# Performance work log

Hardware: AMD Instinct MI355X
Metric: run time of the kernel (lower is better)

The kernel has to match this reference:

```python
import jax, jax.numpy as jnp
from jax import lax
import numpy as np

KS = 5
STRIDE = 4
SCALE = 10.0
PAD = 1        # conv_transpose2d padding (hardcoded in source)
OUT_PAD = 1    # output_padding
DN = ('NCHW', 'OIHW', 'NCHW')


def _same_pad(x, ks, stride):
    # torch same_padding: pad so out = ceil(H/stride)
    H, W = x.shape[-2], x.shape[-1]
    oh = -(-H // stride); ow = -(-W // stride)
    ph = max(0, (oh - 1) * stride + ks - H)
    pw = max(0, (ow - 1) * stride + ks - W)
    return jnp.pad(x, ((0, 0), (0, 0), (ph // 2, ph - ph // 2), (pw // 2, pw - pw // 2)))


def _patches(x, ks, stride):
    # torch extract_image_patches (same padding + unfold), returned as [N, L, C, ks, ks]
    N, C, H, W = x.shape
    oh = -(-H // stride); ow = -(-W // stride)
    xp = _same_pad(x, ks, stride)
    ys = (jnp.arange(oh) * stride)[:, None] + jnp.arange(ks)[None, :]   # [oh, ks]
    xs = (jnp.arange(ow) * stride)[:, None] + jnp.arange(ks)[None, :]   # [ow, ks]
    p = xp[:, :, ys, :][:, :, :, :, xs]   # [N, C, oh, ks, ow, ks]
    return p.transpose(0, 2, 4, 1, 3, 5).reshape(N, oh * ow, C, ks, ks)


def _conv3(x, W, b):
    # BasicBlock: 3x3 conv pad 1 + bias + LeakyReLU(0.01)
    y = lax.conv_general_dilated(x, W, (1, 1), [(1, 1), (1, 1)], dimension_numbers=DN)
    return jax.nn.leaky_relu(y + b[None, :, None, None], 0.01)


def _attend(qp, kp, vp):
    # qp: [C, Hp, Wp] padded query feature; kp: [L, C, ks, ks]; vp: [L, B, ks, ks]
    kmax = jnp.max(jnp.sqrt(jnp.sum(kp * kp, axis=(1, 2, 3))))
    kn = kp / kmax
    w = lax.conv_general_dilated(qp[None], kn, (STRIDE, STRIDE), 'VALID', dimension_numbers=DN)  # [1, L, h, w]
    wn = jax.nn.softmax(w * SCALE, axis=1)
    # conv_transpose2d(wn, vp, stride=4, padding=1, output_padding=1) as lhs-dilated conv
    ker = jnp.flip(vp.transpose(1, 0, 2, 3), (2, 3))  # [B, L, ks, ks]
    lo = KS - 1 - PAD
    hi = KS - 1 - PAD + OUT_PAD
    out = lax.conv_general_dilated(wn, ker, (1, 1), [(lo, hi), (lo, hi)],
                                   lhs_dilation=(STRIDE, STRIDE), dimension_numbers=DN)
    return out[0] / 6.0


def setup_inputs() -> dict:
    key = jax.random.key(0)
    k = jax.random.split(key, 12)
    N, CIN, MID, B = 8, 64, 64, 64
    H, HL = 256, 64
    s = 0.05
    return {
        'ms':   jax.random.normal(k[0], (N, B, HL, HL), jnp.float32),
        'pan':  jax.random.normal(k[1], (N, CIN, H, H), jnp.float32),
        'pan2': jax.random.normal(k[2], (N, CIN, HL, HL), jnp.float32),
        'Wq': jax.random.normal(k[3], (MID, CIN, 3, 3), jnp.float32) * s,
        'bq': jnp.zeros((MID,), jnp.float32),
        'Wk': jax.random.normal(k[4], (MID, CIN, 3, 3), jnp.float32) * s,
        'bk': jnp.zeros((MID,), jnp.float32),
        'Wv': jax.random.normal(k[5], (B, B, 3, 3), jnp.float32) * s,
        'bv': jnp.zeros((B,), jnp.float32),
        'Wr': jax.random.normal(k[6], (B, B, 3, 3), jnp.float32) * s,
        'br': jnp.zeros((B,), jnp.float32),
    }


def reference(ms, pan, pan2, Wq, bq, Wk, bk, Wv, bv, Wr, br):
    k_fea = _conv3(pan2, Wk, bk)               # [N, MID, 64, 64]
    k_patch = _patches(k_fea, KS, STRIDE)      # [N, L=256, MID, 5, 5]
    q_fea = _conv3(pan, Wq, bq)                # [N, MID, 256, 256]
    q_pad = _same_pad(q_fea, KS, STRIDE)       # [N, MID, 257, 257]
    v_fea = _conv3(ms, Wv, bv)                 # [N, B, 64, 64]
    v_patch = _patches(v_fea, KS, STRIDE)      # [N, L, B, 5, 5]
    res = jax.vmap(_attend)(q_pad, k_patch, v_patch)  # [N, B, 256, 256]
    return _conv3(res, Wr, br)
```

## Files before the change

### kernel.cpp

```cpp
#include <hip/hip_runtime.h>
#include <math.h>

#define NB   8
#define CI   64
#define COC  64
#define HQ   256
#define HK   64
#define KS   5
#define LL   256
#define NPAD 1664
#define QP2  (257 * 264)

typedef __attribute__((ext_vector_type(8))) short bf16x8s;
typedef __attribute__((ext_vector_type(4))) float f32x4;

static __device__ __forceinline__ unsigned short f2bf(float f) {
  union { float f; unsigned u; } v; v.f = f;
  unsigned r = v.u + 0x7FFF + ((v.u >> 16) & 1);
  return (unsigned short)(r >> 16);
}
static __device__ __forceinline__ float bf2f(unsigned short h) {
  union { unsigned u; float f; } v; v.u = ((unsigned)h) << 16; return v.f;
}

__global__ void wtrans8_kernel(const float* __restrict__ Wt, float* __restrict__ Wo) {
  const int co = threadIdx.x;
  const int tap = blockIdx.x;
  const int ci = blockIdx.y;
  Wo[(((co >> 3) * 64 + ci) * 9 + tap) * 8 + (co & 7)] = Wt[(co * 64 + ci) * 9 + tap];
}

__global__ void wtrans_mfma(const float* __restrict__ Wt, unsigned short* __restrict__ wimg) {
  const int ch = blockIdx.x;
  const int tap = ch >> 1, cih = ch & 1;
  for (int idx = threadIdx.x; idx < 64 * 40; idx += 256) {
    const int co = idx / 40, s = idx - co * 40;
    unsigned short v = 0;
    if (s < 32) v = f2bf(Wt[((size_t)co * 64 + cih * 32 + s) * 9 + tap]);
    wimg[(size_t)ch * 64 * 40 + idx] = v;
  }
}

__global__ void pad_copy(const float* __restrict__ src, float* __restrict__ dst,
                         int H, int W, int S, int total) {
  const int idx = blockIdx.x * 256 + threadIdx.x;
  if (idx >= total) return;
  const int p = idx / (H * W);
  const int rem = idx - p * H * W;
  const int y = rem / W, x = rem - y * W;
  dst[((size_t)p * (H + 2) + y + 1) * S + x + 1] = src[idx];
}

__global__ void border_zero(float* __restrict__ dst, int H, int W, int S) {
  const int p = blockIdx.x;
  float* b = dst + (size_t)p * (H + 2) * S;
  for (int c = threadIdx.x; c < S; c += 256) {
    b[c] = 0.f;
    b[(size_t)(H + 1) * S + c] = 0.f;
  }
  for (int r = 1 + threadIdx.x; r <= H; r += 256) {
    b[(size_t)r * S] = 0.f;
    b[(size_t)r * S + W + 1] = 0.f;
  }
}

__global__ void pad_rci(const float* __restrict__ src, unsigned short* __restrict__ dst) {
  const int ct = blockIdx.x, g = blockIdx.y, n = blockIdx.z;
  const int c0 = ct * 66;
  __shared__ float t[64 * 68];
  const int jl = threadIdx.x & 63, cg = threadIdx.x >> 6;
  const int row = g - 1;
  const bool rok = (row >= 0 && row < 256);
  for (int ci = cg; ci < 64; ci += 4) {
    #pragma unroll
    for (int jb = 0; jb < 2; ++jb) {
      const int j = jl + jb * 64;
      if (j < 66) {
        const int x = c0 - 1 + j;
        float v = 0.f;
        if (rok && x >= 0 && x < 256)
          v = src[(((size_t)n * 64 + ci) * 256 + row) * 256 + x];
        t[ci * 68 + j] = v;
      }
    }
  }
  __syncthreads();
  const int cil = threadIdx.x & 63, cc = threadIdx.x >> 6;
  unsigned short* db = dst + (((size_t)n * 258 + g) * 264) * 64;
  for (int c = cc; c < 66; c += 4)
    db[(size_t)(c0 + c) * 64 + cil] = f2bf(t[cil * 68 + c]);
}

__global__ void rbz(unsigned short* __restrict__ resbf) {
  const int n = blockIdx.x;
  unsigned short* b = resbf + (size_t)n * 258 * 264 * 64;
  for (int idx = threadIdx.x; idx < 264 * 64; idx += 256) {
    b[idx] = 0;
    b[(size_t)257 * 264 * 64 + idx] = 0;
  }
  for (int idx = threadIdx.x; idx < 256 * 64; idx += 256) {
    const int r = idx >> 6, ci = idx & 63;
    b[((size_t)(r + 1) * 264) * 64 + ci] = 0;
    b[((size_t)(r + 1) * 264 + 257) * 64 + ci] = 0;
  }
}

__global__ void qz(unsigned short* __restrict__ qhi, unsigned short* __restrict__ qlo) {
  const int n = blockIdx.x;
  unsigned short* bh = qhi + (size_t)n * QP2 * 64;
  unsigned short* bl = qlo + (size_t)n * QP2 * 64;
  for (int g = threadIdx.x; g < 4224; g += 256) {
    ((unsigned long long*)(bh + (size_t)256 * 264 * 64))[g] = 0ull;
    ((unsigned long long*)(bl + (size_t)256 * 264 * 64))[g] = 0ull;
  }
  for (int g = threadIdx.x; g < 4096; g += 256) {
    const int r = g >> 4, q = g & 15;
    const size_t off = ((size_t)r * 264 + 256) * 64 + q * 4;
    *(unsigned long long*)(bh + off) = 0ull;
    *(unsigned long long*)(bl + off) = 0ull;
  }
}

__global__ __launch_bounds__(256) void conv3m(
    const unsigned short* __restrict__ inbf,
    const unsigned short* __restrict__ wimg,
    const float* __restrict__ bias,
    float* __restrict__ out, int PS, int RS) {
  const int x0 = blockIdx.x * 64;
  const int y  = blockIdx.y;
  const int n  = blockIdx.z;
  const int tid = threadIdx.x;
  const int lane = tid & 63;
  const int wv = tid >> 6;
  const int col = lane & 15;
  const int kg  = lane >> 4;

  __shared__ unsigned short in_s[3 * 66 * 72];

  {
    const unsigned short* src = inbf + ((size_t)n * 258 + y) * 264 * 64;
    if (tid < 198) {
      const int r = tid / 66, c = tid - r * 66;
      const unsigned short* s = src + ((size_t)r * 264 + x0 + c) * 64;
      unsigned short* d = &in_s[(r * 66 + c) * 72];
      #pragma unroll
      for (int q = 0; q < 8; ++q)
        *(float4*)(d + q * 8) = *(const float4*)(s + q * 8);
    }
  }
  __syncthreads();

  f32x4 acc[4];
  #pragma unroll
  for (int p = 0; p < 4; ++p) acc[p] = (f32x4){0.f, 0.f, 0.f, 0.f};

  const unsigned short* wbase = wimg + ((size_t)(wv * 16 + col)) * 40 + kg * 8;

  #pragma unroll 2
  for (int ch = 0; ch < 18; ++ch) {
    const int tap = ch >> 1, cih = ch & 1;
    const int dy = tap / 3, dx = tap - dy * 3;
    const bf16x8s a = *(const bf16x8s*)(wbase + (size_t)ch * 64 * 40);
    const int cix = cih * 32 + kg * 8;
    #pragma unroll
    for (int p = 0; p < 4; ++p) {
      const int c = p * 16 + col + dx;
      const bf16x8s b = *(const bf16x8s*)&in_s[(dy * 66 + c) * 72 + cix];
      acc[p] = __builtin_amdgcn_mfma_f32_16x16x32_bf16(a, b, acc[p], 0, 0, 0);
    }
  }

  const int cobase = wv * 16 + kg * 4;
  const float4 bb = *(const float4*)&bias[cobase];
  const float bv[4] = {bb.x, bb.y, bb.z, bb.w};
  #pragma unroll
  for (int p = 0; p < 4; ++p) {
    const int x = x0 + p * 16 + col;
    #pragma unroll
    for (int r = 0; r < 4; ++r) {
      float t = acc[p][r] + bv[r];
      t = t > 0.f ? t : 0.01f * t;
      out[(size_t)(n * 64 + cobase + r) * PS + (size_t)y * RS + x] = t;
    }
  }
}

__global__ __launch_bounds__(256) void conv3mq(
    const unsigned short* __restrict__ inbf,
    const unsigned short* __restrict__ wimg,
    const float* __restrict__ bias,
    unsigned short* __restrict__ qhi, unsigned short* __restrict__ qlo) {
  const int x0 = blockIdx.x * 64;
  const int y  = blockIdx.y;
  const int n  = blockIdx.z;
  const int tid = threadIdx.x;
  const int lane = tid & 63;
  const int wv = tid >> 6;
  const int col = lane & 15;
  const int kg  = lane >> 4;

  __shared__ unsigned short in_s[3 * 66 * 72];

  {
    const unsigned short* src = inbf + ((size_t)n * 258 + y) * 264 * 64;
    if (tid < 198) {
      const int r = tid / 66, c = tid - r * 66;
      const unsigned short* s = src + ((size_t)r * 264 + x0 + c) * 64;
      unsigned short* d = &in_s[(r * 66 + c) * 72];
      #pragma unroll
      for (int q = 0; q < 8; ++q)
        *(float4*)(d + q * 8) = *(const float4*)(s + q * 8);
    }
  }
  __syncthreads();

  f32x4 acc[4];
  #pragma unroll
  for (int p = 0; p < 4; ++p) acc[p] = (f32x4){0.f, 0.f, 0.f, 0.f};

  const unsigned short* wbase = wimg + ((size_t)(wv * 16 + col)) * 40 + kg * 8;

  #pragma unroll 2
  for (int ch = 0; ch < 18; ++ch) {
    const int tap = ch >> 1, cih = ch & 1;
    const int dy = tap / 3, dx = tap - dy * 3;
    const bf16x8s a = *(const bf16x8s*)(wbase + (size_t)ch * 64 * 40);
    const int cix = cih * 32 + kg * 8;
    #pragma unroll
    for (int p = 0; p < 4; ++p) {
      const int c = p * 16 + col + dx;
      const bf16x8s b = *(const bf16x8s*)&in_s[(dy * 66 + c) * 72 + cix];
      acc[p] = __builtin_amdgcn_mfma_f32_16x16x32_bf16(a, b, acc[p], 0, 0, 0);
    }
  }

  const int cobase = wv * 16 + kg * 4;
  const float4 bb = *(const float4*)&bias[cobase];
  const float bv[4] = {bb.x, bb.y, bb.z, bb.w};
  unsigned short* hb = qhi + ((size_t)n * 257 + y) * 264 * 64;
  unsigned short* lb = qlo + ((size_t)n * 257 + y) * 264 * 64;
  #pragma unroll
  for (int p = 0; p < 4; ++p) {
    const int x = x0 + p * 16 + col;
    unsigned long long hp = 0, lp = 0;
    #pragma unroll
    for (int r = 0; r < 4; ++r) {
      float t = acc[p][r] + bv[r];
      t = t > 0.f ? t : 0.01f * t;
      const unsigned short h = f2bf(t);
      const unsigned short lo = f2bf(t - bf2f(h));
      hp |= ((unsigned long long)h) << (16 * r);
      lp |= ((unsigned long long)lo) << (16 * r);
    }
    *(unsigned long long*)(hb + (size_t)x * 64 + cobase) = hp;
    *(unsigned long long*)(lb + (size_t)x * 64 + cobase) = lp;
  }
}

__global__ __launch_bounds__(256) void conv3s(
    const float* __restrict__ inp, const float* __restrict__ Wts,
    const float* __restrict__ bias, float* __restrict__ out,
    int H, int Wd, int S, int outPS, int outRS) {
  const int x0 = blockIdx.x * 64;
  const int y0 = blockIdx.y * 8;
  const int z  = blockIdx.z;
  const int n  = z >> 3;
  const int cog = z & 7;
  const int tid = threadIdx.x;
  const int xq = tid & 15;
  const int yt = (tid >> 4) & 7;
  const int cg = tid >> 7;
  const int Hp = H + 2;

  __shared__ float in_s[10 * 72];
  __shared__ float w_s[CI * 9 * 8];

  {
    const float* wbase = Wts + (size_t)cog * (CI * 9 * 8);
    for (int idx = tid; idx < CI * 9 * 2; idx += 256)
      *(float4*)&w_s[idx * 4] = *(const float4*)(wbase + idx * 4);
  }

  float acc[4][4];
  #pragma unroll
  for (int a = 0; a < 4; ++a)
    #pragma unroll
    for (int b = 0; b < 4; ++b) acc[a][b] = 0.f;

  const bool hasA = tid < 180;
  const int arow = tid / 18, ac4 = tid - arow * 18;
  const float* gplane0 = inp + (size_t)(n * CI) * Hp * S;
  const size_t aoff = ((size_t)(y0 + arow)) * S + x0 + ac4 * 4;

  float4 sA = make_float4(0.f, 0.f, 0.f, 0.f);
  if (hasA) sA = *(const float4*)(gplane0 + aoff);

  for (int ci = 0; ci < CI; ++ci) {
    __syncthreads();
    if (hasA) *(float4*)&in_s[arow * 72 + ac4 * 4] = sA;
    if (ci + 1 < CI && hasA)
      sA = *(const float4*)(gplane0 + (size_t)(ci + 1) * Hp * S + aoff);
    __syncthreads();

    float xin[3][8];
    const int cb = xq * 4;
    #pragma unroll
    for (int r = 0; r < 3; ++r) {
      const float4 xa = *(const float4*)&in_s[(yt + r) * 72 + cb];
      const float4 xb = *(const float4*)&in_s[(yt + r) * 72 + cb + 4];
      xin[r][0] = xa.x; xin[r][1] = xa.y; xin[r][2] = xa.z; xin[r][3] = xa.w;
      xin[r][4] = xb.x; xin[r][5] = xb.y; xin[r][6] = xb.z; xin[r][7] = xb.w;
    }

    const float* wci = &w_s[(ci * 9) * 8 + cg * 4];
    #pragma unroll
    for (int ky = 0; ky < 3; ++ky) {
      #pragma unroll
      for (int kx = 0; kx < 3; ++kx) {
        const float4 w4 = *(const float4*)&wci[(ky * 3 + kx) * 8];
        const float wv[4] = {w4.x, w4.y, w4.z, w4.w};
        #pragma unroll
        for (int c = 0; c < 4; ++c)
          #pragma unroll
          for (int dx = 0; dx < 4; ++dx)
            acc[c][dx] = fmaf(wv[c], xin[ky][dx + kx], acc[c][dx]);
      }
    }
  }

  #pragma unroll
  for (int c = 0; c < 4; ++c) {
    const int co = cog * 8 + cg * 4 + c;
    const float bv = bias[co];
    float4 o;
    float t;
    t = acc[c][0] + bv; o.x = t > 0.f ? t : 0.01f * t;
    t = acc[c][1] + bv; o.y = t > 0.f ? t : 0.01f * t;
    t = acc[c][2] + bv; o.z = t > 0.f ? t : 0.01f * t;
    t = acc[c][3] + bv; o.w = t > 0.f ? t : 0.01f * t;
    *(float4*)(out + (size_t)(n * COC + co) * outPS + (size_t)(y0 + yt) * outRS + x0 + xq * 4) = o;
  }
}

__global__ void knorm_kernel(const float* __restrict__ kfea, float* __restrict__ norms) {
  const int l = blockIdx.x, n = blockIdx.y, c = threadIdx.x;
  const int ly = l >> 4, lx = l & 15;
  const float* base = kfea + ((size_t)(n * CI + c) * HK) * HK;
  float ss = 0.f;
  #pragma unroll
  for (int i = 0; i < KS; ++i) {
    const int r = 4 * ly + i;
    if (r >= HK) continue;
    #pragma unroll
    for (int j = 0; j < KS; ++j) {
      const int cc = 4 * lx + j;
      if (cc >= HK) continue;
      const float v = base[r * HK + cc];
      ss = fmaf(v, v, ss);
    }
  }
  for (int off = 32; off; off >>= 1) ss += __shfl_down(ss, off);
  if (c == 0) norms[n * LL + l] = ss;
}

__global__ void kscale_kernel(const float* __restrict__ norms, float* __restrict__ kscale) {
  const int n = blockIdx.x, t = threadIdx.x;
  float v = norms[n * LL + t];
  for (int off = 32; off; off >>= 1) v = fmaxf(v, __shfl_down(v, off));
  __shared__ float red[4];
  if ((t & 63) == 0) red[t >> 6] = v;
  __syncthreads();
  if (t == 0) {
    const float m = fmaxf(fmaxf(red[0], red[1]), fmaxf(red[2], red[3]));
    kscale[n] = 10.0f / sqrtf(m);
  }
}

__global__ void kp_gather2(const float* __restrict__ kfea, const float* __restrict__ kscale,
                           unsigned short* __restrict__ khi, unsigned short* __restrict__ klo) {
  const int tap = blockIdx.x, cih = blockIdx.y, n = blockIdx.z;
  const int s = threadIdx.x & 31, lg = threadIdx.x >> 5;
  const int i = tap / 5, j = tap % 5;
  const float sc = kscale[n];
  const float* kb = kfea + ((size_t)(n * 64 + cih * 32 + s) * 64) * 64;
  const size_t ob = (((size_t)n * 50 + tap * 2 + cih) * 256) * 32;
  for (int lb = 0; lb < 32; ++lb) {
    const int l = lb * 8 + lg;
    const int r = 4 * (l >> 4) + i, c = 4 * (l & 15) + j;
    float v = 0.f;
    if (r < 64 && c < 64) v = kb[r * 64 + c] * sc;
    const unsigned short h = f2bf(v);
    khi[ob + (size_t)l * 32 + s] = h;
    klo[ob + (size_t)l * 32 + s] = f2bf(v - bf2f(h));
  }
}

__global__ __launch_bounds__(256) void qk_mfma(
    const unsigned short* __restrict__ qhi, const unsigned short* __restrict__ qlo,
    const unsigned short* __restrict__ khi, const unsigned short* __restrict__ klo,
    float* __restrict__ scores) {
  const int y = blockIdx.x, n = blockIdx.y;
  const int tid = threadIdx.x;
  const int lane = tid & 63, wv = tid >> 6;
  const int col = lane & 15, kg = lane >> 4;

  f32x4 acc[4][4];
  #pragma unroll
  for (int fm = 0; fm < 4; ++fm)
    #pragma unroll
    for (int fn = 0; fn < 4; ++fn) acc[fm][fn] = (f32x4){0.f, 0.f, 0.f, 0.f};

  const unsigned short* khb = khi + (size_t)n * 50 * 8192;
  const unsigned short* klb = klo + (size_t)n * 50 * 8192;
  const unsigned short* qhb = qhi + (size_t)n * QP2 * 64;
  const unsigned short* qlb = qlo + (size_t)n * QP2 * 64;

  for (int ch = 0; ch < 50; ++ch) {
    const int tap = ch >> 1, cih = ch & 1;
    const int i = tap / 5, j = tap - 5 * i;
    bf16x8s ah[4], al[4];
    #pragma unroll
    for (int fm = 0; fm < 4; ++fm) {
      const size_t qoff = (((size_t)(4 * y + i) * 264) + 4 * (fm * 16 + col) + j) * 64
                        + cih * 32 + kg * 8;
      ah[fm] = *(const bf16x8s*)(qhb + qoff);
      al[fm] = *(const bf16x8s*)(qlb + qoff);
    }
    #pragma unroll
    for (int fn = 0; fn < 4; ++fn) {
      const size_t boff = ((size_t)ch * 256 + wv * 64 + fn * 16 + col) * 32 + kg * 8;
      const bf16x8s bh = *(const bf16x8s*)(khb + boff);
      const bf16x8s bl = *(const bf16x8s*)(klb + boff);
      #pragma unroll
      for (int fm = 0; fm < 4; ++fm) {
        acc[fm][fn] = __builtin_amdgcn_mfma_f32_16x16x32_bf16(ah[fm], bh, acc[fm][fn], 0, 0, 0);
        acc[fm][fn] = __builtin_amdgcn_mfma_f32_16x16x32_bf16(ah[fm], bl, acc[fm][fn], 0, 0, 0);
        acc[fm][fn] = __builtin_amdgcn_mfma_f32_16x16x32_bf16(al[fm], bh, acc[fm][fn], 0, 0, 0);
      }
    }
  }

  float* sb = scores + (size_t)n * 4096 * 256;
  #pragma unroll
  for (int fm = 0; fm < 4; ++fm)
    #pragma unroll
    for (int fn = 0; fn < 4; ++fn)
      #pragma unroll
      for (int r = 0; r < 4; ++r)
        sb[(size_t)(y * 64 + fm * 16 + kg * 4 + r) * 256 + wv * 64 + fn * 16 + col]
            = acc[fm][fn][r];
}

__global__ void softmax_rows(const float* __restrict__ sa, unsigned short* __restrict__ wnbf) {
  const int row = blockIdx.x * 4 + (threadIdx.x >> 6);
  const int lane = threadIdx.x & 63;
  const size_t idx = (size_t)row * 64 + lane;
  const float4 v = ((const float4*)sa)[idx];
  float m = fmaxf(fmaxf(v.x, v.y), fmaxf(v.z, v.w));
  for (int off = 32; off; off >>= 1) m = fmaxf(m, __shfl_xor(m, off));
  float4 e;
  e.x = __expf(v.x - m); e.y = __expf(v.y - m);
  e.z = __expf(v.z - m); e.w = __expf(v.w - m);
  float s = e.x + e.y + e.z + e.w;
  for (int off = 32; off; off >>= 1) s += __shfl_xor(s, off);
  const float inv = 1.0f / s;
  unsigned long long pack = (unsigned long long)f2bf(e.x * inv)
                          | ((unsigned long long)f2bf(e.y * inv) << 16)
                          | ((unsigned long long)f2bf(e.z * inv) << 32)
                          | ((unsigned long long)f2bf(e.w * inv) << 48);
  *(unsigned long long*)(wnbf + idx * 4) = pack;
}

__global__ void vpt_gather(const float* __restrict__ vfea, unsigned short* __restrict__ vpt) {
  const int l4 = threadIdx.x & 63, bj = threadIdx.x >> 6;
  const int bij = blockIdx.x * 4 + bj;
  const int n = blockIdx.y;
  const int ij = bij >> 6, b = bij & 63;
  unsigned short o[4] = {0, 0, 0, 0};
  if (ij < 25) {
    const int i = ij / 5, j = ij % 5;
    const int ly = l4 >> 2;
    const int r = 4 * ly + i;
    if (r < HK) {
      const float* base = vfea + ((size_t)(n * COC + b) * HK + r) * HK;
      #pragma unroll
      for (int e = 0; e < 4; ++e) {
        const int lx = (l4 & 3) * 4 + e;
        const int c = 4 * lx + j;
        if (c < HK) o[e] = f2bf(base[c]);
      }
    }
  }
  unsigned long long pack = (unsigned long long)o[0] | ((unsigned long long)o[1] << 16)
                          | ((unsigned long long)o[2] << 32) | ((unsigned long long)o[3] << 48);
  *(unsigned long long*)(vpt + ((size_t)n * NPAD + bij) * 256 + l4 * 4) = pack;
}

__global__ __launch_bounds__(256) void pv_mfma(
    const unsigned short* __restrict__ wnb, const unsigned short* __restrict__ vpt,
    float* __restrict__ C0) {
  const int nz = blockIdx.z;
  const unsigned short* A = wnb + (size_t)nz * 4096 * 256;
  const unsigned short* B = vpt + (size_t)nz * NPAD * 256;
  float* C = C0 + (size_t)nz * 4096 * NPAD;
  const int m0 = blockIdx.x * 64;
  const int n0 = blockIdx.y * 128;
  const int tid = threadIdx.x;
  const int lane = tid & 63;
  const int wv = tid >> 6;
  const int wm = wv >> 1, wn_ = wv & 1;
  const int col = lane & 15, kg = lane >> 4;

  __shared__ unsigned short A_s[64 * 40];
  __shared__ unsigned short B_s[128 * 40];

  f32x4 acc[2][4];
  #pragma unroll
  for (int fm = 0; fm < 2; ++fm)
    #pragma unroll
    for (int fn = 0; fn < 4; ++fn) acc[fm][fn] = (f32x4){0.f, 0.f, 0.f, 0.f};

  for (int k0 = 0; k0 < 256; k0 += 32) {
    __syncthreads();
    {
      const int row = tid >> 2, q = tid & 3;
      *(float4*)&A_s[row * 40 + q * 8] =
          *(const float4*)&A[(size_t)(m0 + row) * 256 + k0 + q * 8];
    }
    {
      const int row = tid >> 1, hh = tid & 1;
      *(float4*)&B_s[row * 40 + hh * 16] =
          *(const float4*)&B[(size_t)(n0 + row) * 256 + k0 + hh * 16];
      *(float4*)&B_s[row * 40 + hh * 16 + 8] =
          *(const float4*)&B[(size_t)(n0 + row) * 256 + k0 + hh * 16 + 8];
    }
    __syncthreads();

    bf16x8s a[2], b[4];
    #pragma unroll
    for (int fm = 0; fm < 2; ++fm)
      a[fm] = *(const bf16x8s*)&A_s[(wm * 32 + fm * 16 + col) * 40 + kg * 8];
    #pragma unroll
    for (int fn = 0; fn < 4; ++fn)
      b[fn] = *(const bf16x8s*)&B_s[(wn_ * 64 + fn * 16 + col) * 40 + kg * 8];
    #pragma unroll
    for (int fm = 0; fm < 2; ++fm)
      #pragma unroll
      for (int fn = 0; fn < 4; ++fn)
        acc[fm][fn] = __builtin_amdgcn_mfma_f32_16x16x32_bf16(a[fm], b[fn], acc[fm][fn], 0, 0, 0);
  }

  #pragma unroll
  for (int fm = 0; fm < 2; ++fm) {
    #pragma unroll
    for (int fn = 0; fn < 4; ++fn) {
      const int cg = n0 + wn_ * 64 + fn * 16 + col;
      #pragma unroll
      for (int r = 0; r < 4; ++r) {
        const int rg = m0 + wm * 32 + fm * 16 + kg * 4 + r;
        C[(size_t)rg * NPAD + cg] = acc[fm][fn][r];
      }
    }
  }
}

__global__ __launch_bounds__(256) void u_scatter(
    const float* __restrict__ U0, unsigned short* __restrict__ resbf, int n0) {
  const int n = n0 + blockIdx.z;
  const float* U = U0 + (size_t)blockIdx.z * 4096 * NPAD;
  const int y = blockIdx.y;
  const int xt = blockIdx.x;
  const int tid = threadIdx.x;
  __shared__ float t_lds[64][65];
  const int ym = (y + 1) >> 2, yr = (y + 1) & 3;
  const bool v0 = (ym < 64);
  const bool v1 = (yr == 0 && ym >= 1);
  const int b = tid & 63, xg = tid >> 6;
  for (int xi = 0; xi < 16; ++xi) {
    const int x = xt * 64 + xg * 16 + xi;
    const int xm = (x + 1) >> 2, xr = (x + 1) & 3;
    const bool u0 = (xm < 64);
    const bool u1 = (xr == 0 && xm >= 1);
    float s = 0.f;
    if (v0) {
      const size_t rb = (size_t)(ym * 64) * NPAD;
      if (u0) s += U[rb + (size_t)xm * NPAD + (yr * 5 + xr) * 64 + b];
      if (u1) s += U[rb + (size_t)(xm - 1) * NPAD + (yr * 5 + 4) * 64 + b];
    }
    if (v1) {
      const size_t rb = (size_t)((ym - 1) * 64) * NPAD;
      if (u0) s += U[rb + (size_t)xm * NPAD + (4 * 5 + xr) * 64 + b];
      if (u1) s += U[rb + (size_t)(xm - 1) * NPAD + (4 * 5 + 4) * 64 + b];
    }
    t_lds[xg * 16 + xi][b] = s * (1.0f / 6.0f);
  }
  __syncthreads();
  unsigned short* db = resbf + (((size_t)n * 258 + (y + 1)) * 264) * 64;
  for (int xi = 0; xi < 16; ++xi) {
    const int x = xg * 16 + xi;
    db[(size_t)(xt * 64 + x + 1) * 64 + b] = f2bf(t_lds[x][b]);
  }
}

extern "C" void kernel_launch(void* const* d_in, const int* in_sizes, int n_in,
                              void* d_out, int out_size, void* d_ws, size_t ws_size,
                              hipStream_t stream) {
  const float* ms   = (const float*)d_in[0];
  const float* pan  = (const float*)d_in[1];
  const float* pan2 = (const float*)d_in[2];
  const float* Wq   = (const float*)d_in[3];
  const float* bq   = (const float*)d_in[4];
  const float* Wk   = (const float*)d_in[5];
  const float* bk   = (const float*)d_in[6];
  const float* Wv   = (const float*)d_in[7];
  const float* bv   = (const float*)d_in[8];
  const float* Wr   = (const float*)d_in[9];
  const float* br   = (const float*)d_in[10];
  float* out = (float*)d_out;

  float* ws = (float*)d_ws;
  const size_t SZ_QP  = (size_t)NB * CI * QP2;
  const size_t SZ_K   = (size_t)NB * CI * HK * HK;
  const size_t SZ_WN  = (size_t)NB * 64 * 64 * LL;
  const size_t SZ_VPT = (size_t)NB * NPAD * 256 / 2;
  const size_t SZ_KP  = (size_t)NB * 50 * 256 * 32;
  const size_t SZ_PS  = (size_t)NB * CI * 66 * 72;
  const size_t SZ_WI  = 23040;
  const size_t SZ_U1  = (size_t)4096 * NPAD;
  const size_t SZ_UA  = (size_t)NB * SZ_U1;

  float* q_pad   = ws;
  float* k_fea   = q_pad + SZ_QP;
  float* v_fea   = k_fea + SZ_K;
  float* wnbf_f  = v_fea + SZ_K;
  float* vptbf_f = wnbf_f + SZ_WN / 2;
  float* kp      = vptbf_f + SZ_VPT;
  float* norms   = kp + SZ_KP;
  float* kscale  = norms + NB * LL;
  float* wtk     = kscale + 64;
  float* wtv     = wtk + 36864;
  float* wimgqf  = wtv + 36864;
  float* wimgrf  = wimgqf + SZ_WI;
  float* ms_pad  = wimgrf + SZ_WI;
  float* pan2pad = ms_pad + SZ_PS;
  float* tail    = pan2pad + SZ_PS;

  unsigned short* qhi  = (unsigned short*)q_pad;
  unsigned short* qlo  = qhi + (size_t)NB * QP2 * 64;
  unsigned short* khi  = (unsigned short*)kp;
  unsigned short* klo  = khi + (size_t)NB * 50 * 256 * 32;
  unsigned short* wimgq = (unsigned short*)wimgqf;
  unsigned short* wimgr = (unsigned short*)wimgrf;
  unsigned short* wnbf  = (unsigned short*)wnbf_f;
  unsigned short* vptbf = (unsigned short*)vptbf_f;
  unsigned short* panbf = (unsigned short*)tail;
  float* scores  = tail;
  float* U       = tail;
  unsigned short* resbf = (unsigned short*)q_pad;

  const size_t base_elems = (size_t)(tail - ws);
  const bool batched = ws_size >= (base_elems + SZ_UA) * sizeof(float);

  wtrans8_kernel<<<dim3(9, 64), 64, 0, stream>>>(Wk, wtk);
  wtrans8_kernel<<<dim3(9, 64), 64, 0, stream>>>(Wv, wtv);
  wtrans_mfma<<<dim3(18), 256, 0, stream>>>(Wq, wimgq);
  wtrans_mfma<<<dim3(18), 256, 0, stream>>>(Wr, wimgr);

  {
    const int totS = NB * CI * HK * HK;
    pad_copy<<<dim3((totS + 255) / 256), 256, 0, stream>>>(ms, ms_pad, HK, HK, 72, totS);
    pad_copy<<<dim3((totS + 255) / 256), 256, 0, stream>>>(pan2, pan2pad, HK, HK, 72, totS);
    border_zero<<<dim3(NB * CI), 256, 0, stream>>>(ms_pad, HK, HK, 72);
    border_zero<<<dim3(NB * CI), 256, 0, stream>>>(pan2pad, HK, HK, 72);
    pad_rci<<<dim3(4, 258, NB), 256, 0, stream>>>(pan, panbf);
  }

  conv3s<<<dim3(HK / 64, HK / 8, NB * 8), 256, 0, stream>>>(pan2pad, wtk, bk, k_fea, HK, HK, 72, HK * HK, HK);
  conv3s<<<dim3(HK / 64, HK / 8, NB * 8), 256, 0, stream>>>(ms_pad,  wtv, bv, v_fea, HK, HK, 72, HK * HK, HK);
  conv3mq<<<dim3(4, 256, NB), 256, 0, stream>>>(panbf, wimgq, bq, qhi, qlo);
  qz<<<dim3(NB), 256, 0, stream>>>(qhi, qlo);

  knorm_kernel<<<dim3(LL, NB), 64, 0, stream>>>(k_fea, norms);
  kscale_kernel<<<NB, 256, 0, stream>>>(norms, kscale);

  kp_gather2<<<dim3(25, 2, NB), 256, 0, stream>>>(k_fea, kscale, khi, klo);

  qk_mfma<<<dim3(64, NB), 256, 0, stream>>>(qhi, qlo, khi, klo, scores);
  softmax_rows<<<dim3(8192), 256, 0, stream>>>(scores, wnbf);

  rbz<<<dim3(NB), 256, 0, stream>>>(resbf);

  vpt_gather<<<dim3(NPAD / 4, NB), 256, 0, stream>>>(v_fea, vptbf);

  if (batched) {
    pv_mfma<<<dim3(64, 13, NB), 256, 0, stream>>>(wnbf, vptbf, U);
    u_scatter<<<dim3(4, HQ, NB), 256, 0, stream>>>(U, resbf, 0);
  } else {
    for (int n = 0; n < NB; ++n) {
      pv_mfma<<<dim3(64, 13, 1), 256, 0, stream>>>(wnbf + (size_t)n * 4096 * 256,
                                                   vptbf + (size_t)n * NPAD * 256, U);
      u_scatter<<<dim3(4, HQ, 1), 256, 0, stream>>>(U, resbf, n);
    }
  }

  conv3m<<<dim3(4, 256, NB), 256, 0, stream>>>(resbf, wimgr, br, out, HQ * HQ, HQ);
}
```

Baseline: 777.1 us.

## Fuse softmax into QK MFMA kernel and store PV output as bf16

The QK score kernel now runs 512 threads per block, with each wave covering 32 of the 256 keys. It computes the row softmax in-register, using shuffle and LDS reductions across waves, and writes bf16 weights directly. This removes the fp32 scores round trip and the separate softmax launch. Separately, the PV GEMM output U is stored as bf16 instead of fp32, halving its write and read traffic in u_scatter. This adds extra rounding of intermediate sums, and the larger batched workspace condition now holds more easily.

```diff
diff --git a/kernel.cpp b/kernel.cpp
--- a/kernel.cpp
+++ b/kernel.cpp
@@ -395,20 +395,23 @@
   }
 }
 
-__global__ __launch_bounds__(256) void qk_mfma(
+__global__ __launch_bounds__(512) void qk_fused(
     const unsigned short* __restrict__ qhi, const unsigned short* __restrict__ qlo,
     const unsigned short* __restrict__ khi, const unsigned short* __restrict__ klo,
-    float* __restrict__ scores) {
-  const int y = blockIdx.x, n = blockIdx.y;
+    unsigned short* __restrict__ wnbf) {
+  const int yb = blockIdx.x, n = blockIdx.y;
   const int tid = threadIdx.x;
   const int lane = tid & 63, wv = tid >> 6;
   const int col = lane & 15, kg = lane >> 4;
 
-  f32x4 acc[4][4];
+  __shared__ float red[64][9];
+  __shared__ float redm[64];
+
+  f32x4 acc[4][2];
   #pragma unroll
   for (int fm = 0; fm < 4; ++fm)
     #pragma unroll
-    for (int fn = 0; fn < 4; ++fn) acc[fm][fn] = (f32x4){0.f, 0.f, 0.f, 0.f};
+    for (int fn = 0; fn < 2; ++fn) acc[fm][fn] = (f32x4){0.f, 0.f, 0.f, 0.f};
 
   const unsigned short* khb = khi + (size_t)n * 50 * 8192;
   const unsigned short* klb = klo + (size_t)n * 50 * 8192;
@@ -421,14 +424,14 @@
     bf16x8s ah[4], al[4];
     #pragma unroll
     for (int fm = 0; fm < 4; ++fm) {
-      const size_t qoff = (((size_t)(4 * y + i) * 264) + 4 * (fm * 16 + col) + j) * 64
+      const size_t qoff = (((size_t)(4 * yb + i) * 264) + 4 * (fm * 16 + col) + j) * 64
                         + cih * 32 + kg * 8;
       ah[fm] = *(const bf16x8s*)(qhb + qoff);
       al[fm] = *(const bf16x8s*)(qlb + qoff);
     }
     #pragma unroll
-    for (int fn = 0; fn < 4; ++fn) {
-      const size_t boff = ((size_t)ch * 256 + wv * 64 + fn * 16 + col) * 32 + kg * 8;
+    for (int fn = 0; fn < 2; ++fn) {
+      const size_t boff = ((size_t)ch * 256 + wv * 32 + fn * 16 + col) * 32 + kg * 8;
       const bf16x8s bh = *(const bf16x8s*)(khb + boff);
       const bf16x8s bl = *(const bf16x8s*)(klb + boff);
       #pragma unroll
@@ -440,35 +443,55 @@
     }
   }
 
-  float* sb = scores + (size_t)n * 4096 * 256;
   #pragma unroll
   for (int fm = 0; fm < 4; ++fm)
     #pragma unroll
-    for (int fn = 0; fn < 4; ++fn)
-      #pragma unroll
-      for (int r = 0; r < 4; ++r)
-        sb[(size_t)(y * 64 + fm * 16 + kg * 4 + r) * 256 + wv * 64 + fn * 16 + col]
-            = acc[fm][fn][r];
-}
-
-__global__ void softmax_rows(const float* __restrict__ sa, unsigned short* __restrict__ wnbf) {
-  const int row = blockIdx.x * 4 + (threadIdx.x >> 6);
-  const int lane = threadIdx.x & 63;
-  const size_t idx = (size_t)row * 64 + lane;
-  const float4 v = ((const float4*)sa)[idx];
-  float m = fmaxf(fmaxf(v.x, v.y), fmaxf(v.z, v.w));
-  for (int off = 32; off; off >>= 1) m = fmaxf(m, __shfl_xor(m, off));
-  float4 e;
-  e.x = __expf(v.x - m); e.y = __expf(v.y - m);
-  e.z = __expf(v.z - m); e.w = __expf(v.w - m);
-  float s = e.x + e.y + e.z + e.w;
-  for (int off = 32; off; off >>= 1) s += __shfl_xor(s, off);
-  const float inv = 1.0f / s;
-  unsigned long long pack = (unsigned long long)f2bf(e.x * inv)
-                          | ((unsigned long long)f2bf(e.y * inv) << 16)
-                          | ((unsigned long long)f2bf(e.z * inv) << 32)
-                          | ((unsigned long long)f2bf(e.w * inv) << 48);
-  *(unsigned long long*)(wnbf + idx * 4) = pack;
+    for (int r = 0; r < 4; ++r) {
+      float m = fmaxf(acc[fm][0][r], acc[fm][1][r]);
+      #pragma unroll
+      for (int off = 1; off < 16; off <<= 1) m = fmaxf(m, __shfl_xor(m, off));
+      if (col == 0) red[fm * 16 + kg * 4 + r][wv] = m;
+    }
+  __syncthreads();
+  if (tid < 64) {
+    float bm = red[tid][0];
+    #pragma unroll
+    for (int w = 1; w < 8; ++w) bm = fmaxf(bm, red[tid][w]);
+    redm[tid] = bm;
+  }
+  __syncthreads();
+  #pragma unroll
+  for (int fm = 0; fm < 4; ++fm)
+    #pragma unroll
+    for (int r = 0; r < 4; ++r) {
+      const float bm = redm[fm * 16 + kg * 4 + r];
+      const float e0 = __expf(acc[fm][0][r] - bm);
+      const float e1 = __expf(acc[fm][1][r] - bm);
+      acc[fm][0][r] = e0;
+      acc[fm][1][r] = e1;
+      float s = e0 + e1;
+      #pragma unroll
+      for (int off = 1; off < 16; off <<= 1) s += __shfl_xor(s, off);
+      if (col == 0) red[fm * 16 + kg * 4 + r][wv] = s;
+    }
+  __syncthreads();
+  if (tid < 64) {
+    float s = red[tid][0];
+    #pragma unroll
+    for (int w = 1; w < 8; ++w) s += red[tid][w];
+    redm[tid] = 1.0f / s;
+  }
+  __syncthreads();
+  unsigned short* wb = wnbf + ((size_t)n * 4096 + (size_t)yb * 64) * 256;
+  #pragma unroll
+  for (int fm = 0; fm < 4; ++fm)
+    #pragma unroll
+    for (int r = 0; r < 4; ++r) {
+      const int q = fm * 16 + kg * 4 + r;
+      const float inv = redm[q];
+      wb[(size_t)q * 256 + wv * 32 + col]      = f2bf(acc[fm][0][r] * inv);
+      wb[(size_t)q * 256 + wv * 32 + 16 + col] = f2bf(acc[fm][1][r] * inv);
+    }
 }
 
 __global__ void vpt_gather(const float* __restrict__ vfea, unsigned short* __restrict__ vpt) {
@@ -498,11 +521,11 @@
 
 __global__ __launch_bounds__(256) void pv_mfma(
     const unsigned short* __restrict__ wnb, const unsigned short* __restrict__ vpt,
-    float* __restrict__ C0) {
+    unsigned short* __restrict__ C0) {
   const int nz = blockIdx.z;
   const unsigned short* A = wnb + (size_t)nz * 4096 * 256;
   const unsigned short* B = vpt + (size_t)nz * NPAD * 256;
-  float* C = C0 + (size_t)nz * 4096 * NPAD;
+  unsigned short* C = C0 + (size_t)nz * 4096 * NPAD;
   const int m0 = blockIdx.x * 64;
   const int n0 = blockIdx.y * 128;
   const int tid = threadIdx.x;
@@ -558,16 +581,16 @@
       #pragma unroll
       for (int r = 0; r < 4; ++r) {
         const int rg = m0 + wm * 32 + fm * 16 + kg * 4 + r;
-        C[(size_t)rg * NPAD + cg] = acc[fm][fn][r];
+        C[(size_t)rg * NPAD + cg] = f2bf(acc[fm][fn][r]);
       }
     }
   }
 }
 
 __global__ __launch_bounds__(256) void u_scatter(
-    const float* __restrict__ U0, unsigned short* __restrict__ resbf, int n0) {
+    const unsigned short* __restrict__ U0, unsigned short* __restrict__ resbf, int n0) {
   const int n = n0 + blockIdx.z;
-  const float* U = U0 + (size_t)blockIdx.z * 4096 * NPAD;
+  const unsigned short* U = U0 + (size_t)blockIdx.z * 4096 * NPAD;
   const int y = blockIdx.y;
   const int xt = blockIdx.x;
   const int tid = threadIdx.x;
@@ -584,13 +607,13 @@
     float s = 0.f;
     if (v0) {
       const size_t rb = (size_t)(ym * 64) * NPAD;
-      if (u0) s += U[rb + (size_t)xm * NPAD + (yr * 5 + xr) * 64 + b];
-      if (u1) s += U[rb + (size_t)(xm - 1) * NPAD + (yr * 5 + 4) * 64 + b];
+      if (u0) s += bf2f(U[rb + (size_t)xm * NPAD + (yr * 5 + xr) * 64 + b]);
+      if (u1) s += bf2f(U[rb + (size_t)(xm - 1) * NPAD + (yr * 5 + 4) * 64 + b]);
     }
     if (v1) {
       const size_t rb = (size_t)((ym - 1) * 64) * NPAD;
-      if (u0) s += U[rb + (size_t)xm * NPAD + (4 * 5 + xr) * 64 + b];
-      if (u1) s += U[rb + (size_t)(xm - 1) * NPAD + (4 * 5 + 4) * 64 + b];
+      if (u0) s += bf2f(U[rb + (size_t)xm * NPAD + (4 * 5 + xr) * 64 + b]);
+      if (u1) s += bf2f(U[rb + (size_t)(xm - 1) * NPAD + (4 * 5 + 4) * 64 + b]);
     }
     t_lds[xg * 16 + xi][b] = s * (1.0f / 6.0f);
   }
@@ -626,8 +649,8 @@
   const size_t SZ_KP  = (size_t)NB * 50 * 256 * 32;
   const size_t SZ_PS  = (size_t)NB * CI * 66 * 72;
   const size_t SZ_WI  = 23040;
-  const size_t SZ_U1  = (size_t)4096 * NPAD;
-  const size_t SZ_UA  = (size_t)NB * SZ_U1;
+  const size_t SZ_U1F = (size_t)4096 * NPAD / 2;
+  const size_t SZ_UAF = (size_t)NB * SZ_U1F;
 
   float* q_pad   = ws;
   float* k_fea   = q_pad + SZ_QP;
@@ -654,12 +677,11 @@
   unsigned short* wnbf  = (unsigned short*)wnbf_f;
   unsigned short* vptbf = (unsigned short*)vptbf_f;
   unsigned short* panbf = (unsigned short*)tail;
-  float* scores  = tail;
-  float* U       = tail;
+  unsigned short* U     = (unsigned short*)tail;
   unsigned short* resbf = (unsigned short*)q_pad;
 
   const size_t base_elems = (size_t)(tail - ws);
-  const bool batched = ws_size >= (base_elems + SZ_UA) * sizeof(float);
+  const bool batched = ws_size >= (base_elems + SZ_UAF) * sizeof(float);
 
   wtrans8_kernel<<<dim3(9, 64), 64, 0, stream>>>(Wk, wtk);
   wtrans8_kernel<<<dim3(9, 64), 64, 0, stream>>>(Wv, wtv);
@@ -685,8 +707,7 @@
 
   kp_gather2<<<dim3(25, 2, NB), 256, 0, stream>>>(k_fea, kscale, khi, klo);
 
-  qk_mfma<<<dim3(64, NB), 256, 0, stream>>>(qhi, qlo, khi, klo, scores);
-  softmax_rows<<<dim3(8192), 256, 0, stream>>>(scores, wnbf);
+  qk_fused<<<dim3(64, NB), 512, 0, stream>>>(qhi, qlo, khi, klo, wnbf);
 
   rbz<<<dim3(NB), 256, 0, stream>>>(resbf);
 
```

Result: slower. 813.6 us (+4.7%).
